# Performance work log

Hardware: AMD Instinct MI355X
Metric: run time of the kernel (lower is better)

The kernel has to match this reference:

```python
import jax, jax.numpy as jnp
import numpy as np

BN_EPS = 1e-5


def setup_inputs() -> dict:
    key = jax.random.key(0)
    ks = jax.random.split(key, 8)
    B, T, D, Tu, Dout, M = 32, 4096, 128, 512, 64, 8
    feats = jax.random.normal(ks[0], (B, T, D), dtype=jnp.float32)
    # integer time-window ids stored in channel 0 of x; pin 0 and Tu-1 so
    # tw_uniq = arange(0, Tu) exactly (no -99 padding) for every batch row
    tw = jax.random.randint(ks[1], (B, T), 0, Tu)
    tw = tw.at[:, 0].set(0).at[:, 1].set(Tu - 1)
    x = jnp.concatenate([tw[..., None].astype(jnp.float32), feats], axis=-1)
    mask = jax.random.uniform(ks[2], (B, T, 1)) < 0.9
    mask = mask.at[:, :2].set(True)  # keep pinned min/max entries valid
    tw_uniq = jnp.broadcast_to(jnp.arange(Tu, dtype=jnp.float32)[None, :, None], (B, Tu, 1))
    bn_gamma = jax.random.uniform(ks[3], (D,), jnp.float32, 0.5, 1.5)
    bn_beta = 0.1 * jax.random.normal(ks[4], (D,), dtype=jnp.float32)
    bn_mean = jnp.zeros((D,), jnp.float32)
    bn_var = jnp.ones((D,), jnp.float32)
    conv_w = jax.random.normal(ks[5], (Dout, D), dtype=jnp.float32) / np.float32(np.sqrt(D))
    conv_b = jnp.zeros((Dout,), jnp.float32)
    fc_w = jax.random.normal(ks[6], (M, Dout), dtype=jnp.float32) / np.float32(np.sqrt(Dout))
    fc_b = jnp.zeros((M,), jnp.float32)
    return dict(x=x, mask=mask, tw_uniq=tw_uniq, bn_gamma=bn_gamma, bn_beta=bn_beta,
                bn_mean=bn_mean, bn_var=bn_var, conv_w=conv_w, conv_b=conv_b,
                fc_w=fc_w, fc_b=fc_b)


def reference(x, mask, tw_uniq, bn_gamma, bn_beta, bn_mean, bn_var,
              conv_w, conv_b, fc_w, fc_b):
    # --- TimeWindowPooling (segment-max form of the dense expand+where+amax) ---
    # torch computes amax_T(where(tw==tw_uniq & mask, x, 0)) -> max(0, group max).
    # Equivalent: scatter-max of mask-zeroed values into a zeros-initialized
    # (B, Tu, D) buffer, avoiding the O(B*T*Tu*D) blowup.
    tw = x[..., 0]           # (B, T) integer-valued, detached in torch
    feats = x[..., 1:]       # (B, T, D)
    B, T, D = feats.shape
    Tu = tw_uniq.shape[1]
    u0 = tw_uniq[:, 0, 0]    # per-batch window minimum
    idx = jnp.clip((tw - u0[:, None]).astype(jnp.int32), 0, Tu - 1)  # (B, T)
    vals = jnp.where(mask, feats, 0.0)  # masked rows contribute 0 == init value
    hidden = jnp.zeros((B, Tu, D), feats.dtype).at[jnp.arange(B)[:, None], idx].max(vals)
    # --- mlp_down: BatchNorm1d (inference stats) + 1x1 Conv1d over channels ---
    h = (hidden - bn_mean) * jax.lax.rsqrt(bn_var + BN_EPS) * bn_gamma + bn_beta
    h = jnp.einsum('bud,od->buo', h, conv_w) + conv_b  # (B, Tu, Dout)
    # --- fc_out ---
    return jnp.einsum('buo,mo->bum', h, fc_w) + fc_b   # (B, Tu, M)
```

## Files before the change

### kernel.cpp

```cpp
#include <hip/hip_runtime.h>

#define B_   32
#define T_   4096
#define D_   128
#define TU   512
#define M_   8
#define O_   64
#define HW   64
#define TILE (TU * HW)
#define TSL  1024
#define BN_EPS 1e-5f

typedef float f4u __attribute__((ext_vector_type(4), aligned(4)));



__global__ __launch_bounds__(1024) void scatter_kernel(
    const float* __restrict__ x,
    const int*   __restrict__ mask,
    const float* __restrict__ tw_uniq,
    float*       __restrict__ wsF) {
    __shared__ unsigned hid[TILE];
    __shared__ int uidxs[TSL];
    const int i = blockIdx.x;
    const int b = (i & 7) + 8 * ((i >> 3) & 3);
    const int r = i >> 5;
    const int h = r >> 2;
    const int q = r & 3;
    const int tid = threadIdx.x;
    const int tb = q * TSL;

    const float* xb = x + (size_t)b * T_ * (D_ + 1);

    const float twf = xb[(size_t)(tb + tid) * (D_ + 1)];
    const int   mk  = mask[b * T_ + tb + tid];
    const float u0  = tw_uniq[b * TU];

#pragma unroll
    for (int c = 0; c < TILE / 4096; ++c)
        *(float4*)&hid[c * 4096 + tid * 4] = make_float4(0.f, 0.f, 0.f, 0.f);

    uidxs[tid] = mk ? min(max((int)(twf - u0), 0), TU - 1) : -1;
    __syncthreads();

    const int rloc = tid >> 4;
    const int lq   = tid & 15;
    const float* fb = xb + 1 + h * HW + lq * 4;
    for (int it = 0; it < TSL / 64 / 8; ++it) {
        f4u fv[8];
        int uu[8];
#pragma unroll
        for (int j = 0; j < 8; ++j) {
            const int t = tb + (it * 8 + j) * 64 + rloc;
            fv[j] = *(const f4u*)(fb + (size_t)t * (D_ + 1));
        }
#pragma unroll
        for (int j = 0; j < 8; ++j)
            uu[j] = uidxs[(it * 8 + j) * 64 + rloc];
#pragma unroll
        for (int j = 0; j < 8; ++j) {
            if (uu[j] >= 0) {
                unsigned* hp = &hid[(uu[j] << 6) + ((lq ^ (uu[j] & 15)) << 2)];
                if (fv[j].x > 0.f) atomicMax(hp + 0, __float_as_uint(fv[j].x));
                if (fv[j].y > 0.f) atomicMax(hp + 1, __float_as_uint(fv[j].y));
                if (fv[j].z > 0.f) atomicMax(hp + 2, __float_as_uint(fv[j].z));
                if (fv[j].w > 0.f) atomicMax(hp + 3, __float_as_uint(fv[j].w));
            }
        }
    }
    __syncthreads();

    float* tp = wsF + (size_t)(((b * 2 + h) << 2) + q) * TILE;
#pragma unroll
    for (int c = 0; c < TILE / 4096; ++c)
        *(float4*)(tp + c * 4096 + tid * 4) = *(const float4*)&hid[c * 4096 + tid * 4];
}

__global__ __launch_bounds__(1024) void merge_mm_kernel(
    const float* __restrict__ bn_gamma, const float* __restrict__ bn_beta,
    const float* __restrict__ bn_mean,  const float* __restrict__ bn_var,
    const float* __restrict__ conv_w,   const float* __restrict__ conv_b,
    const float* __restrict__ fc_w,     const float* __restrict__ fc_b,
    const float* __restrict__ wsF, float* __restrict__ out) {
    __shared__ float wsm[M_ * D_];
    __shared__ float tmp[M_ * D_];
    __shared__ float biasc[M_];
    const int j = blockIdx.x;
    const int b  = (j & 7) + 8 * ((j >> 3) & 3);
    const int uc = j >> 5;
    const int tid = threadIdx.x;

    {
        const int m = tid >> 7, d = tid & (D_ - 1);
        float wraw = 0.f;
        for (int o = 0; o < O_; ++o) wraw += fc_w[m * O_ + o] * conv_w[o * D_ + d];
        const float sc = bn_gamma[d] * rsqrtf(bn_var[d] + BN_EPS);
        const float sh = bn_beta[d] - bn_mean[d] * sc;
        wsm[tid] = wraw * sc;
        tmp[tid] = wraw * sh;
    }
    __syncthreads();
    if (tid < M_) {
        float s = fc_b[tid];
        for (int o = 0; o < O_; ++o) s += fc_w[tid * O_ + o] * conv_b[o];
        for (int d = 0; d < D_; ++d) s += tmp[tid * D_ + d];
        biasc[tid] = s;
    }
    __syncthreads();

    const int w    = tid >> 6;
    const int lane = tid & 63;
    const int half = lane >> 5;
    const int l5   = lane & 31;
    const int u    = uc * 32 + w * 2 + half;
    const int hh   = l5 >> 4;
    const int dq   = l5 & 15;
    const int slot = dq ^ (u & 15);

    const float* tp = wsF + (size_t)((b * 2 + hh) << 2) * TILE + u * HW + slot * 4;
    const float4 v0 = *(const float4*)(tp);
    const float4 v1 = *(const float4*)(tp + TILE);
    const float4 v2 = *(const float4*)(tp + 2 * TILE);
    const float4 v3 = *(const float4*)(tp + 3 * TILE);
    const float a0 = fmaxf(fmaxf(v0.x, v1.x), fmaxf(v2.x, v3.x));
    const float a1 = fmaxf(fmaxf(v0.y, v1.y), fmaxf(v2.y, v3.y));
    const float a2 = fmaxf(fmaxf(v0.z, v1.z), fmaxf(v2.z, v3.z));
    const float a3 = fmaxf(fmaxf(v0.w, v1.w), fmaxf(v2.w, v3.w));

    const int db = l5 << 2;
    float p0, p1, p2, p3, p4, p5, p6, p7;
#define PDOT(mm) (a0 * wsm[(mm) * D_ + db] + a1 * wsm[(mm) * D_ + db + 1] + \
                  a2 * wsm[(mm) * D_ + db + 2] + a3 * wsm[(mm) * D_ + db + 3])
    p0 = PDOT(0); p1 = PDOT(1); p2 = PDOT(2); p3 = PDOT(3);
    p4 = PDOT(4); p5 = PDOT(5); p6 = PDOT(6); p7 = PDOT(7);
#undef PDOT
#pragma unroll
    for (int off = 1; off < 32; off <<= 1) {
        p0 += __shfl_xor(p0, off); p1 += __shfl_xor(p1, off);
        p2 += __shfl_xor(p2, off); p3 += __shfl_xor(p3, off);
        p4 += __shfl_xor(p4, off); p5 += __shfl_xor(p5, off);
        p6 += __shfl_xor(p6, off); p7 += __shfl_xor(p7, off);
    }
    if (l5 == 0) {
        float* op = out + ((size_t)(b * TU + u)) * M_;
        *(float4*)(op)     = make_float4(p0 + biasc[0], p1 + biasc[1],
                                         p2 + biasc[2], p3 + biasc[3]);
        *(float4*)(op + 4) = make_float4(p4 + biasc[4], p5 + biasc[5],
                                         p6 + biasc[6], p7 + biasc[7]);
    }
}

extern "C" void kernel_launch(void* const* d_in, const int* in_sizes, int n_in,
                              void* d_out, int out_size, void* d_ws, size_t ws_size,
                              hipStream_t stream) {
    const float* x        = (const float*)d_in[0];
    const int*   mask     = (const int*)  d_in[1];
    const float* tw_uniq  = (const float*)d_in[2];
    const float* bn_gamma = (const float*)d_in[3];
    const float* bn_beta  = (const float*)d_in[4];
    const float* bn_mean  = (const float*)d_in[5];
    const float* bn_var   = (const float*)d_in[6];
    const float* conv_w   = (const float*)d_in[7];
    const float* conv_b   = (const float*)d_in[8];
    const float* fc_w     = (const float*)d_in[9];
    const float* fc_b     = (const float*)d_in[10];
    float* wsF = (float*)d_ws;
    float* out = (float*)d_out;

    scatter_kernel<<<256, 1024, 0, stream>>>(x, mask, tw_uniq, wsF);
    merge_mm_kernel<<<512, 1024, 0, stream>>>(
        bn_gamma, bn_beta, bn_mean, bn_var,
        conv_w, conv_b, fc_w, fc_b, wsF, out);
}
```

Baseline: 136.4 us.

## Fuse scatter-max and matmul into one kernel with per-chunk compacted row lists

```diff
diff --git a/kernel.cpp b/kernel.cpp
--- a/kernel.cpp
+++ b/kernel.cpp
@@ -6,89 +6,51 @@
 #define TU   512
 #define M_   8
 #define O_   64
-#define HW   64
-#define TILE (TU * HW)
-#define TSL  1024
+#define UCH  64
+#define PADW 132
+#define LCAP 2048
 #define BN_EPS 1e-5f
 
 typedef float f4u __attribute__((ext_vector_type(4), aligned(4)));
 
-
-
-__global__ __launch_bounds__(1024) void scatter_kernel(
+__global__ __launch_bounds__(1024) void fused_kernel(
     const float* __restrict__ x,
     const int*   __restrict__ mask,
     const float* __restrict__ tw_uniq,
-    float*       __restrict__ wsF) {
-    __shared__ unsigned hid[TILE];
-    __shared__ int uidxs[TSL];
-    const int i = blockIdx.x;
-    const int b = (i & 7) + 8 * ((i >> 3) & 3);
-    const int r = i >> 5;
-    const int h = r >> 2;
-    const int q = r & 3;
+    const float* __restrict__ bn_gamma,
+    const float* __restrict__ bn_beta,
+    const float* __restrict__ bn_mean,
+    const float* __restrict__ bn_var,
+    const float* __restrict__ conv_w,
+    const float* __restrict__ conv_b,
+    const float* __restrict__ fc_w,
+    const float* __restrict__ fc_b,
+    float*       __restrict__ out) {
+    __shared__ unsigned hid[UCH * PADW];
+    __shared__ int   list[LCAP];
+    __shared__ float wsm[M_ * D_];
+    __shared__ float tmp[M_ * D_];
+    __shared__ float biasc[M_];
+    __shared__ int   nlist;
+    const int i   = blockIdx.x;
+    const int b   = (i & 7) + 8 * ((i >> 3) & 3);
+    const int uc  = i >> 5;
     const int tid = threadIdx.x;
-    const int tb = q * TSL;
+    const int u_lo = uc * UCH;
 
     const float* xb = x + (size_t)b * T_ * (D_ + 1);
 
-    const float twf = xb[(size_t)(tb + tid) * (D_ + 1)];
-    const int   mk  = mask[b * T_ + tb + tid];
-    const float u0  = tw_uniq[b * TU];
+    float twf[4]; int mk[4];
+#pragma unroll
+    for (int k = 0; k < 4; ++k) {
+        const int t = k * 1024 + tid;
+        twf[k] = xb[(size_t)t * (D_ + 1)];
+        mk[k]  = mask[b * T_ + t];
+    }
+    const float u0 = tw_uniq[b * TU];
 
-#pragma unroll
-    for (int c = 0; c < TILE / 4096; ++c)
-        *(float4*)&hid[c * 4096 + tid * 4] = make_float4(0.f, 0.f, 0.f, 0.f);
-
-    uidxs[tid] = mk ? min(max((int)(twf - u0), 0), TU - 1) : -1;
-    __syncthreads();
-
-    const int rloc = tid >> 4;
-    const int lq   = tid & 15;
-    const float* fb = xb + 1 + h * HW + lq * 4;
-    for (int it = 0; it < TSL / 64 / 8; ++it) {
-        f4u fv[8];
-        int uu[8];
-#pragma unroll
-        for (int j = 0; j < 8; ++j) {
-            const int t = tb + (it * 8 + j) * 64 + rloc;
-            fv[j] = *(const f4u*)(fb + (size_t)t * (D_ + 1));
-        }
-#pragma unroll
-        for (int j = 0; j < 8; ++j)
-            uu[j] = uidxs[(it * 8 + j) * 64 + rloc];
-#pragma unroll
-        for (int j = 0; j < 8; ++j) {
-            if (uu[j] >= 0) {
-                unsigned* hp = &hid[(uu[j] << 6) + ((lq ^ (uu[j] & 15)) << 2)];
-                if (fv[j].x > 0.f) atomicMax(hp + 0, __float_as_uint(fv[j].x));
-                if (fv[j].y > 0.f) atomicMax(hp + 1, __float_as_uint(fv[j].y));
-                if (fv[j].z > 0.f) atomicMax(hp + 2, __float_as_uint(fv[j].z));
-                if (fv[j].w > 0.f) atomicMax(hp + 3, __float_as_uint(fv[j].w));
-            }
-        }
-    }
-    __syncthreads();
-
-    float* tp = wsF + (size_t)(((b * 2 + h) << 2) + q) * TILE;
-#pragma unroll
-    for (int c = 0; c < TILE / 4096; ++c)
-        *(float4*)(tp + c * 4096 + tid * 4) = *(const float4*)&hid[c * 4096 + tid * 4];
-}
-
-__global__ __launch_bounds__(1024) void merge_mm_kernel(
-    const float* __restrict__ bn_gamma, const float* __restrict__ bn_beta,
-    const float* __restrict__ bn_mean,  const float* __restrict__ bn_var,
-    const float* __restrict__ conv_w,   const float* __restrict__ conv_b,
-    const float* __restrict__ fc_w,     const float* __restrict__ fc_b,
-    const float* __restrict__ wsF, float* __restrict__ out) {
-    __shared__ float wsm[M_ * D_];
-    __shared__ float tmp[M_ * D_];
-    __shared__ float biasc[M_];
-    const int j = blockIdx.x;
-    const int b  = (j & 7) + 8 * ((j >> 3) & 3);
-    const int uc = j >> 5;
-    const int tid = threadIdx.x;
+    if (tid == 0) nlist = 0;
+    for (int p = tid; p < UCH * PADW; p += 1024) hid[p] = 0u;
 
     {
         const int m = tid >> 7, d = tid & (D_ - 1);
@@ -106,47 +68,85 @@
         for (int d = 0; d < D_; ++d) s += tmp[tid * D_ + d];
         biasc[tid] = s;
     }
+
+    const int lane = tid & 63;
+#pragma unroll
+    for (int k = 0; k < 4; ++k) {
+        const int t = k * 1024 + tid;
+        const int u = min(max((int)(twf[k] - u0), 0), TU - 1);
+        const int ul = u - u_lo;
+        const bool want = (mk[k] != 0) && (ul >= 0) && (ul < UCH);
+        const unsigned long long bal = __ballot(want);
+        if (bal) {
+            const int cnt = __popcll(bal);
+            const int leader = __ffsll((long long)bal) - 1;
+            int base = 0;
+            if (lane == leader) base = atomicAdd(&nlist, cnt);
+            base = __shfl(base, leader);
+            if (want) {
+                const int pos = base + __popcll(bal & ((1ull << lane) - 1ull));
+                if (pos < LCAP) list[pos] = t | (ul << 12);
+            }
+        }
+    }
+    __syncthreads();
+    const int n = min(nlist, LCAP);
+
+    const int hw = tid >> 5;
+    const int l5 = tid & 31;
+    for (int be = 0; be < n; be += 32 * 8) {
+        f4u fv[8]; int uu[8], ok[8];
+#pragma unroll
+        for (int k = 0; k < 8; ++k) {
+            const int e = be + k * 32 + hw;
+            ok[k] = (e < n);
+            const int ent = list[ok[k] ? e : 0];
+            uu[k] = ent >> 12;
+            fv[k] = *(const f4u*)(xb + (size_t)(ent & 4095) * (D_ + 1) + 1 + (l5 << 2));
+        }
+#pragma unroll
+        for (int k = 0; k < 8; ++k) {
+            if (ok[k]) {
+                unsigned* hp = &hid[uu[k] * PADW + (l5 << 2)];
+                if (fv[k].x > 0.f) atomicMax(hp + 0, __float_as_uint(fv[k].x));
+                if (fv[k].y > 0.f) atomicMax(hp + 1, __float_as_uint(fv[k].y));
+                if (fv[k].z > 0.f) atomicMax(hp + 2, __float_as_uint(fv[k].z));
+                if (fv[k].w > 0.f) atomicMax(hp + 3, __float_as_uint(fv[k].w));
+            }
+        }
+    }
     __syncthreads();
 
-    const int w    = tid >> 6;
-    const int lane = tid & 63;
-    const int half = lane >> 5;
-    const int l5   = lane & 31;
-    const int u    = uc * 32 + w * 2 + half;
-    const int hh   = l5 >> 4;
-    const int dq   = l5 & 15;
-    const int slot = dq ^ (u & 15);
-
-    const float* tp = wsF + (size_t)((b * 2 + hh) << 2) * TILE + u * HW + slot * 4;
-    const float4 v0 = *(const float4*)(tp);
-    const float4 v1 = *(const float4*)(tp + TILE);
-    const float4 v2 = *(const float4*)(tp + 2 * TILE);
-    const float4 v3 = *(const float4*)(tp + 3 * TILE);
-    const float a0 = fmaxf(fmaxf(v0.x, v1.x), fmaxf(v2.x, v3.x));
-    const float a1 = fmaxf(fmaxf(v0.y, v1.y), fmaxf(v2.y, v3.y));
-    const float a2 = fmaxf(fmaxf(v0.z, v1.z), fmaxf(v2.z, v3.z));
-    const float a3 = fmaxf(fmaxf(v0.w, v1.w), fmaxf(v2.w, v3.w));
-
-    const int db = l5 << 2;
-    float p0, p1, p2, p3, p4, p5, p6, p7;
+#pragma unroll
+    for (int it = 0; it < 2; ++it) {
+        const int ul = hw + it * 32;
+        const int u  = u_lo + ul;
+        const uint4 hb = *(const uint4*)&hid[ul * PADW + (l5 << 2)];
+        const float a0 = __uint_as_float(hb.x);
+        const float a1 = __uint_as_float(hb.y);
+        const float a2 = __uint_as_float(hb.z);
+        const float a3 = __uint_as_float(hb.w);
+        const int db = l5 << 2;
+        float p0, p1, p2, p3, p4, p5, p6, p7;
 #define PDOT(mm) (a0 * wsm[(mm) * D_ + db] + a1 * wsm[(mm) * D_ + db + 1] + \
                   a2 * wsm[(mm) * D_ + db + 2] + a3 * wsm[(mm) * D_ + db + 3])
-    p0 = PDOT(0); p1 = PDOT(1); p2 = PDOT(2); p3 = PDOT(3);
-    p4 = PDOT(4); p5 = PDOT(5); p6 = PDOT(6); p7 = PDOT(7);
+        p0 = PDOT(0); p1 = PDOT(1); p2 = PDOT(2); p3 = PDOT(3);
+        p4 = PDOT(4); p5 = PDOT(5); p6 = PDOT(6); p7 = PDOT(7);
 #undef PDOT
 #pragma unroll
-    for (int off = 1; off < 32; off <<= 1) {
-        p0 += __shfl_xor(p0, off); p1 += __shfl_xor(p1, off);
-        p2 += __shfl_xor(p2, off); p3 += __shfl_xor(p3, off);
-        p4 += __shfl_xor(p4, off); p5 += __shfl_xor(p5, off);
-        p6 += __shfl_xor(p6, off); p7 += __shfl_xor(p7, off);
-    }
-    if (l5 == 0) {
-        float* op = out + ((size_t)(b * TU + u)) * M_;
-        *(float4*)(op)     = make_float4(p0 + biasc[0], p1 + biasc[1],
-                                         p2 + biasc[2], p3 + biasc[3]);
-        *(float4*)(op + 4) = make_float4(p4 + biasc[4], p5 + biasc[5],
-                                         p6 + biasc[6], p7 + biasc[7]);
+        for (int off = 1; off < 32; off <<= 1) {
+            p0 += __shfl_xor(p0, off); p1 += __shfl_xor(p1, off);
+            p2 += __shfl_xor(p2, off); p3 += __shfl_xor(p3, off);
+            p4 += __shfl_xor(p4, off); p5 += __shfl_xor(p5, off);
+            p6 += __shfl_xor(p6, off); p7 += __shfl_xor(p7, off);
+        }
+        if (l5 == 0) {
+            float* op = out + ((size_t)(b * TU + u)) * M_;
+            *(float4*)(op)     = make_float4(p0 + biasc[0], p1 + biasc[1],
+                                             p2 + biasc[2], p3 + biasc[3]);
+            *(float4*)(op + 4) = make_float4(p4 + biasc[4], p5 + biasc[5],
+                                             p6 + biasc[6], p7 + biasc[7]);
+        }
     }
 }
 
@@ -164,11 +164,9 @@
     const float* conv_b   = (const float*)d_in[8];
     const float* fc_w     = (const float*)d_in[9];
     const float* fc_b     = (const float*)d_in[10];
-    float* wsF = (float*)d_ws;
     float* out = (float*)d_out;
 
-    scatter_kernel<<<256, 1024, 0, stream>>>(x, mask, tw_uniq, wsF);
-    merge_mm_kernel<<<512, 1024, 0, stream>>>(
-        bn_gamma, bn_beta, bn_mean, bn_var,
-        conv_w, conv_b, fc_w, fc_b, wsF, out);
+    fused_kernel<<<256, 1024, 0, stream>>>(
+        x, mask, tw_uniq, bn_gamma, bn_beta, bn_mean, bn_var,
+        conv_w, conv_b, fc_w, fc_b, out);
 }
```

New measurement: 125.9 us. 1.08x faster.
